# Kernel optimization log

Hardware: AMD Instinct MI355X
Metric: run time of the kernel (lower is better)

Reference implementation:

```python
import jax, jax.numpy as jnp
import numpy as np

TOP_K = 2
N_EXPERTS = 8
ALPHA = 0.1


def setup_inputs() -> dict:
    key = jax.random.key(0)
    k1, k2 = jax.random.split(key)
    hidden_states = jax.random.normal(k1, (4, 8192, 2048), dtype=jnp.float32)
    weight = jax.random.normal(k2, (N_EXPERTS, 2048), dtype=jnp.float32) * (1.0 / np.sqrt(2048))
    return {"hidden_states": hidden_states, "weight": weight}


def reference(hidden_states, weight):
    B, S, H = hidden_states.shape
    E, K = N_EXPERTS, TOP_K
    x = hidden_states.reshape(-1, H)                      # [B*S, H]
    logits = jnp.einsum('th,eh->te', x, weight)           # [B*S, E]
    scores = jax.nn.softmax(logits, axis=-1)
    topk_weight, topk_idx = jax.lax.top_k(scores, K)      # [B*S, K]
    # normalize top-k probs (norm_topk_prob=True, top_k>1)
    topk_weight = topk_weight / (topk_weight.sum(axis=-1, keepdims=True) + 1e-20)
    # seq_aux load-balancing loss (training path)
    idx = topk_idx.reshape(B, S * K)                      # [B, S*K]
    ce = jnp.zeros((B, E), dtype=scores.dtype).at[jnp.arange(B)[:, None], idx].add(1.0)
    ce = ce / (S * K / E)
    pi = scores.reshape(B, S, E).mean(axis=1)             # [B, E]
    aux_loss = (ce * pi).sum(axis=1).mean() * ALPHA
    return topk_idx, topk_weight, aux_loss
```

## Files before the change

kernel.cpp:

```cpp
#include <hip/hip_runtime.h>

#define T_TOK   32768
#define HDIM    2048
#define NEXP    8
#define SEQ     8192
#define NBATCH  4
#define ALPHA   0.1f

#define BLOCK   512
#define TPB     64
#define NBLK    (T_TOK / TPB)
#define H4      (HDIM / 4)
#define NJ      (H4 / 16)

__global__ __launch_bounds__(64) void init_ws_kernel(float* ws) {
    ws[threadIdx.x] = 0.0f;
}

__global__ __launch_bounds__(BLOCK, 4) void gate_kernel(
    const float* __restrict__ x,
    const float* __restrict__ w,
    float* __restrict__ out_idx,
    float* __restrict__ out_wt,
    float* __restrict__ ws)
{
    __shared__ float4 wlds[NEXP * H4];
    __shared__ float sacc[16];

    const int tid  = threadIdx.x;
    const int wid  = tid >> 6;
    const int lane = tid & 63;
    const int grp  = lane >> 4;
    const int col  = lane & 15;

    const float4* w4 = (const float4*)w;
    #pragma unroll
    for (int i = 0; i < 8; ++i)
        wlds[tid + i * BLOCK] = w4[tid + i * BLOCK];
    if (tid < 16) sacc[tid] = 0.0f;
    __syncthreads();

    const int tok0 = blockIdx.x * TPB + wid * 8 + grp * 2;
    const int b    = (blockIdx.x * TPB) / SEQ;

    const float4* xp0 = (const float4*)x + (size_t)tok0 * H4 + col;
    const float4* xp1 = xp0 + H4;

    float acc[2][NEXP];
    #pragma unroll
    for (int t = 0; t < 2; ++t)
        #pragma unroll
        for (int e = 0; e < NEXP; ++e) acc[t][e] = 0.0f;

    float4 xb0[2], xb1[2];
    float4 wA[4], wB[4];

    xb0[0] = xp0[0];        xb0[1] = xp1[0];
    xb1[0] = xp0[16];       xb1[1] = xp1[16];
    #pragma unroll
    for (int e = 0; e < 4; ++e) wA[e] = wlds[e * H4 + col];
    #pragma unroll
    for (int e = 0; e < 4; ++e) wB[e] = wlds[(e + 4) * H4 + col];

#define FMA4(ACC, XV, WV)                      \
    ACC = fmaf((XV).x, (WV).x, ACC);           \
    ACC = fmaf((XV).y, (WV).y, ACC);           \
    ACC = fmaf((XV).z, (WV).z, ACC);           \
    ACC = fmaf((XV).w, (WV).w, ACC);

#define COMPUTE_HALF(XB, WH, EBASE)            \
    _Pragma("unroll")                          \
    for (int e = 0; e < 4; ++e) {              \
        const float4 wv = WH[e];               \
        FMA4(acc[0][(EBASE) + e], XB[0], wv);  \
        FMA4(acc[1][(EBASE) + e], XB[1], wv);  \
    }

    #pragma unroll 1
    for (int jj = 0; jj < NJ - 2; jj += 2) {
        COMPUTE_HALF(xb0, wA, 0)
        #pragma unroll
        for (int e = 0; e < 4; ++e) wA[e] = wlds[e * H4 + (jj + 1) * 16 + col];
        COMPUTE_HALF(xb0, wB, 4)
        #pragma unroll
        for (int e = 0; e < 4; ++e) wB[e] = wlds[(e + 4) * H4 + (jj + 1) * 16 + col];
        xb0[0] = xp0[(jj + 2) * 16];
        xb0[1] = xp1[(jj + 2) * 16];

        COMPUTE_HALF(xb1, wA, 0)
        #pragma unroll
        for (int e = 0; e < 4; ++e) wA[e] = wlds[e * H4 + (jj + 2) * 16 + col];
        COMPUTE_HALF(xb1, wB, 4)
        #pragma unroll
        for (int e = 0; e < 4; ++e) wB[e] = wlds[(e + 4) * H4 + (jj + 2) * 16 + col];
        xb1[0] = xp0[(jj + 3) * 16];
        xb1[1] = xp1[(jj + 3) * 16];
    }

    {
        COMPUTE_HALF(xb0, wA, 0)
        #pragma unroll
        for (int e = 0; e < 4; ++e) wA[e] = wlds[e * H4 + (NJ - 1) * 16 + col];
        COMPUTE_HALF(xb0, wB, 4)
        #pragma unroll
        for (int e = 0; e < 4; ++e) wB[e] = wlds[(e + 4) * H4 + (NJ - 1) * 16 + col];
        COMPUTE_HALF(xb1, wA, 0)
        COMPUTE_HALF(xb1, wB, 4)
    }

    #pragma unroll
    for (int t = 0; t < 2; ++t)
        #pragma unroll
        for (int e = 0; e < NEXP; ++e) {
            float v = acc[t][e];
            v += __shfl_xor(v, 1);
            v += __shfl_xor(v, 2);
            v += __shfl_xor(v, 4);
            v += __shfl_xor(v, 8);
            acc[t][e] = v;
        }

    const int t = col & 1;
    float l[NEXP];
    #pragma unroll
    for (int e = 0; e < NEXP; ++e) l[e] = acc[t][e];

    float mx = l[0];
    #pragma unroll
    for (int e = 1; e < NEXP; ++e) mx = fmaxf(mx, l[e]);

    float p[NEXP];
    float psum = 0.0f;
    #pragma unroll
    for (int e = 0; e < NEXP; ++e) { p[e] = __expf(l[e] - mx); psum += p[e]; }
    const float inv = 1.0f / psum;
    float s[NEXP];
    #pragma unroll
    for (int e = 0; e < NEXP; ++e) s[e] = p[e] * inv;

    float s1 = s[0]; int i1 = 0;
    #pragma unroll
    for (int e = 1; e < NEXP; ++e) if (s[e] > s1) { s1 = s[e]; i1 = e; }
    float s2 = -1.0f; int i2 = 0;
    #pragma unroll
    for (int e = 0; e < NEXP; ++e) if (e != i1 && s[e] > s2) { s2 = s[e]; i2 = e; }

    const float wsum = s1 + s2 + 1e-20f;
    const float w1 = s1 / wsum;
    const float w2 = s2 / wsum;

    if (col < 2) {
        const int tok = tok0 + t;
        ((float2*)out_idx)[tok] = make_float2((float)i1, (float)i2);
        ((float2*)out_wt)[tok]  = make_float2(w1, w2);
    }

    const float sel = (col < 2) ? 1.0f : 0.0f;
    #pragma unroll
    for (int e = 0; e < NEXP; ++e) {
        float pi = s[e] * sel;
        float ce = (((i1 == e) ? 1.0f : 0.0f) + ((i2 == e) ? 1.0f : 0.0f)) * sel;
        pi += __shfl_xor(pi, 1);  ce += __shfl_xor(ce, 1);
        pi += __shfl_xor(pi, 16); ce += __shfl_xor(ce, 16);
        pi += __shfl_xor(pi, 32); ce += __shfl_xor(ce, 32);
        if (lane == 0) {
            atomicAdd(&sacc[e], pi);
            atomicAdd(&sacc[8 + e], ce);
        }
    }
    __syncthreads();
    if (tid < 8)
        atomicAdd(&ws[b * NEXP + tid], sacc[tid]);
    else if (tid < 16)
        atomicAdd(&ws[32 + b * NEXP + (tid - 8)], sacc[tid]);
}

__global__ __launch_bounds__(64) void finalize_kernel(const float* __restrict__ ws,
                                                      float* __restrict__ out_aux) {
    if (threadIdx.x == 0) {
        float aux = 0.0f;
        #pragma unroll
        for (int b = 0; b < NBATCH; ++b) {
            float dot = 0.0f;
            #pragma unroll
            for (int e = 0; e < NEXP; ++e) {
                const float ce = ws[32 + b * NEXP + e] * ((float)NEXP / (float)(SEQ * 2));
                const float pi = ws[b * NEXP + e] / (float)SEQ;
                dot = fmaf(ce, pi, dot);
            }
            aux += dot;
        }
        out_aux[0] = aux * (1.0f / NBATCH) * ALPHA;
    }
}

extern "C" void kernel_launch(void* const* d_in, const int* in_sizes, int n_in,
                              void* d_out, int out_size, void* d_ws, size_t ws_size,
                              hipStream_t stream) {
    const float* x = (const float*)d_in[0];
    const float* w = (const float*)d_in[1];

    float* out     = (float*)d_out;
    float* out_idx = out;
    float* out_wt  = out + 2 * T_TOK;
    float* out_aux = out + 4 * T_TOK;
    float* ws      = (float*)d_ws;

    init_ws_kernel<<<1, 64, 0, stream>>>(ws);
    gate_kernel<<<NBLK, BLOCK, 0, stream>>>(x, w, out_idx, out_wt, ws);
    finalize_kernel<<<1, 64, 0, stream>>>(ws, out_aux);
}
```

Before: 63.51 us.

## Retile gate GEMV to 32 lanes per group with 4 tokens each

```diff
diff --git a/kernel.cpp b/kernel.cpp
--- a/kernel.cpp
+++ b/kernel.cpp
@@ -11,7 +11,7 @@
 #define TPB     64
 #define NBLK    (T_TOK / TPB)
 #define H4      (HDIM / 4)
-#define NJ      (H4 / 16)
+#define NJ2     (H4 / 32)
 
 __global__ __launch_bounds__(64) void init_ws_kernel(float* ws) {
     ws[threadIdx.x] = 0.0f;
@@ -30,8 +30,8 @@
     const int tid  = threadIdx.x;
     const int wid  = tid >> 6;
     const int lane = tid & 63;
-    const int grp  = lane >> 4;
-    const int col  = lane & 15;
+    const int grp  = lane >> 5;
+    const int col  = lane & 31;
 
     const float4* w4 = (const float4*)w;
     #pragma unroll
@@ -40,23 +40,31 @@
     if (tid < 16) sacc[tid] = 0.0f;
     __syncthreads();
 
-    const int tok0 = blockIdx.x * TPB + wid * 8 + grp * 2;
+    const int tok0 = blockIdx.x * TPB + wid * 8 + grp * 4;
     const int b    = (blockIdx.x * TPB) / SEQ;
 
     const float4* xp0 = (const float4*)x + (size_t)tok0 * H4 + col;
     const float4* xp1 = xp0 + H4;
-
-    float acc[2][NEXP];
-    #pragma unroll
-    for (int t = 0; t < 2; ++t)
-        #pragma unroll
-        for (int e = 0; e < NEXP; ++e) acc[t][e] = 0.0f;
-
-    float4 xb0[2], xb1[2];
+    const float4* xp2 = xp0 + 2 * H4;
+    const float4* xp3 = xp0 + 3 * H4;
+
+    float acc[4][NEXP];
+    #pragma unroll
+    for (int m = 0; m < 4; ++m)
+        #pragma unroll
+        for (int e = 0; e < NEXP; ++e) acc[m][e] = 0.0f;
+
+    float4 xb0[4], xb1[4];
     float4 wA[4], wB[4];
 
-    xb0[0] = xp0[0];        xb0[1] = xp1[0];
-    xb1[0] = xp0[16];       xb1[1] = xp1[16];
+#define LOADX(DST, J)                          \
+    DST[0] = xp0[(J) * 32];                    \
+    DST[1] = xp1[(J) * 32];                    \
+    DST[2] = xp2[(J) * 32];                    \
+    DST[3] = xp3[(J) * 32];
+
+    LOADX(xb0, 0)
+    LOADX(xb1, 1)
     #pragma unroll
     for (int e = 0; e < 4; ++e) wA[e] = wlds[e * H4 + col];
     #pragma unroll
@@ -74,53 +82,54 @@
         const float4 wv = WH[e];               \
         FMA4(acc[0][(EBASE) + e], XB[0], wv);  \
         FMA4(acc[1][(EBASE) + e], XB[1], wv);  \
+        FMA4(acc[2][(EBASE) + e], XB[2], wv);  \
+        FMA4(acc[3][(EBASE) + e], XB[3], wv);  \
     }
 
     #pragma unroll 1
-    for (int jj = 0; jj < NJ - 2; jj += 2) {
+    for (int jj = 0; jj < NJ2 - 2; jj += 2) {
         COMPUTE_HALF(xb0, wA, 0)
         #pragma unroll
-        for (int e = 0; e < 4; ++e) wA[e] = wlds[e * H4 + (jj + 1) * 16 + col];
+        for (int e = 0; e < 4; ++e) wA[e] = wlds[e * H4 + (jj + 1) * 32 + col];
         COMPUTE_HALF(xb0, wB, 4)
         #pragma unroll
-        for (int e = 0; e < 4; ++e) wB[e] = wlds[(e + 4) * H4 + (jj + 1) * 16 + col];
-        xb0[0] = xp0[(jj + 2) * 16];
-        xb0[1] = xp1[(jj + 2) * 16];
+        for (int e = 0; e < 4; ++e) wB[e] = wlds[(e + 4) * H4 + (jj + 1) * 32 + col];
+        LOADX(xb0, jj + 2)
 
         COMPUTE_HALF(xb1, wA, 0)
         #pragma unroll
-        for (int e = 0; e < 4; ++e) wA[e] = wlds[e * H4 + (jj + 2) * 16 + col];
+        for (int e = 0; e < 4; ++e) wA[e] = wlds[e * H4 + (jj + 2) * 32 + col];
         COMPUTE_HALF(xb1, wB, 4)
         #pragma unroll
-        for (int e = 0; e < 4; ++e) wB[e] = wlds[(e + 4) * H4 + (jj + 2) * 16 + col];
-        xb1[0] = xp0[(jj + 3) * 16];
-        xb1[1] = xp1[(jj + 3) * 16];
+        for (int e = 0; e < 4; ++e) wB[e] = wlds[(e + 4) * H4 + (jj + 2) * 32 + col];
+        LOADX(xb1, jj + 3)
     }
 
     {
         COMPUTE_HALF(xb0, wA, 0)
         #pragma unroll
-        for (int e = 0; e < 4; ++e) wA[e] = wlds[e * H4 + (NJ - 1) * 16 + col];
+        for (int e = 0; e < 4; ++e) wA[e] = wlds[e * H4 + (NJ2 - 1) * 32 + col];
         COMPUTE_HALF(xb0, wB, 4)
         #pragma unroll
-        for (int e = 0; e < 4; ++e) wB[e] = wlds[(e + 4) * H4 + (NJ - 1) * 16 + col];
+        for (int e = 0; e < 4; ++e) wB[e] = wlds[(e + 4) * H4 + (NJ2 - 1) * 32 + col];
         COMPUTE_HALF(xb1, wA, 0)
         COMPUTE_HALF(xb1, wB, 4)
     }
 
     #pragma unroll
-    for (int t = 0; t < 2; ++t)
+    for (int m = 0; m < 4; ++m)
         #pragma unroll
         for (int e = 0; e < NEXP; ++e) {
-            float v = acc[t][e];
+            float v = acc[m][e];
             v += __shfl_xor(v, 1);
             v += __shfl_xor(v, 2);
             v += __shfl_xor(v, 4);
             v += __shfl_xor(v, 8);
-            acc[t][e] = v;
+            v += __shfl_xor(v, 16);
+            acc[m][e] = v;
         }
 
-    const int t = col & 1;
+    const int t = col & 3;
     float l[NEXP];
     #pragma unroll
     for (int e = 0; e < NEXP; ++e) l[e] = acc[t][e];
@@ -149,19 +158,19 @@
     const float w1 = s1 / wsum;
     const float w2 = s2 / wsum;
 
-    if (col < 2) {
+    if (col < 4) {
         const int tok = tok0 + t;
         ((float2*)out_idx)[tok] = make_float2((float)i1, (float)i2);
         ((float2*)out_wt)[tok]  = make_float2(w1, w2);
     }
 
-    const float sel = (col < 2) ? 1.0f : 0.0f;
+    const float sel = (col < 4) ? 1.0f : 0.0f;
     #pragma unroll
     for (int e = 0; e < NEXP; ++e) {
         float pi = s[e] * sel;
         float ce = (((i1 == e) ? 1.0f : 0.0f) + ((i2 == e) ? 1.0f : 0.0f)) * sel;
         pi += __shfl_xor(pi, 1);  ce += __shfl_xor(ce, 1);
-        pi += __shfl_xor(pi, 16); ce += __shfl_xor(ce, 16);
+        pi += __shfl_xor(pi, 2);  ce += __shfl_xor(ce, 2);
         pi += __shfl_xor(pi, 32); ce += __shfl_xor(ce, 32);
         if (lane == 0) {
             atomicAdd(&sacc[e], pi);
```

New measurement: 182.5 us. 187% more time.

## Replace global atomics with per-block partials and drop workspace init kernel

Applied to the files above, without the earlier changes.

```diff
diff --git a/kernel.cpp b/kernel.cpp
--- a/kernel.cpp
+++ b/kernel.cpp
@@ -10,14 +10,11 @@
 #define BLOCK   512
 #define TPB     64
 #define NBLK    (T_TOK / TPB)
+#define BPB     (SEQ / TPB)
 #define H4      (HDIM / 4)
 #define NJ      (H4 / 16)
 
-__global__ __launch_bounds__(64) void init_ws_kernel(float* ws) {
-    ws[threadIdx.x] = 0.0f;
-}
-
-__global__ __launch_bounds__(BLOCK, 4) void gate_kernel(
+__global__ __launch_bounds__(BLOCK, 2) void gate_kernel(
     const float* __restrict__ x,
     const float* __restrict__ w,
     float* __restrict__ out_idx,
@@ -41,7 +38,6 @@
     __syncthreads();
 
     const int tok0 = blockIdx.x * TPB + wid * 8 + grp * 2;
-    const int b    = (blockIdx.x * TPB) / SEQ;
 
     const float4* xp0 = (const float4*)x + (size_t)tok0 * H4 + col;
     const float4* xp1 = xp0 + H4;
@@ -120,10 +116,11 @@
             acc[t][e] = v;
         }
 
-    const int t = col & 1;
+    const bool selLo = (col & 1) != 0;
     float l[NEXP];
     #pragma unroll
-    for (int e = 0; e < NEXP; ++e) l[e] = acc[t][e];
+    for (int e = 0; e < NEXP; ++e)
+        l[e] = selLo ? acc[1][e] : acc[0][e];
 
     float mx = l[0];
     #pragma unroll
@@ -150,7 +147,7 @@
     const float w2 = s2 / wsum;
 
     if (col < 2) {
-        const int tok = tok0 + t;
+        const int tok = tok0 + (col & 1);
         ((float2*)out_idx)[tok] = make_float2((float)i1, (float)i2);
         ((float2*)out_wt)[tok]  = make_float2(w1, w2);
     }
@@ -169,23 +166,35 @@
         }
     }
     __syncthreads();
-    if (tid < 8)
-        atomicAdd(&ws[b * NEXP + tid], sacc[tid]);
-    else if (tid < 16)
-        atomicAdd(&ws[32 + b * NEXP + (tid - 8)], sacc[tid]);
+    if (tid < 16)
+        ws[blockIdx.x * 16 + tid] = sacc[tid];
 }
 
-__global__ __launch_bounds__(64) void finalize_kernel(const float* __restrict__ ws,
-                                                      float* __restrict__ out_aux) {
-    if (threadIdx.x == 0) {
+__global__ __launch_bounds__(256) void finalize_kernel(const float* __restrict__ ws,
+                                                       float* __restrict__ out_aux) {
+    __shared__ float sfin[NBATCH][16];
+    const int t    = threadIdx.x;
+    const int b    = t >> 6;
+    const int lane = t & 63;
+    const int slot = lane & 15;
+
+    float v = 0.0f;
+    for (int j = lane >> 4; j < BPB; j += 4)
+        v += ws[(b * BPB + j) * 16 + slot];
+    v += __shfl_xor(v, 16);
+    v += __shfl_xor(v, 32);
+    if (lane < 16) sfin[b][slot] = v;
+    __syncthreads();
+
+    if (t == 0) {
         float aux = 0.0f;
         #pragma unroll
-        for (int b = 0; b < NBATCH; ++b) {
+        for (int bb = 0; bb < NBATCH; ++bb) {
             float dot = 0.0f;
             #pragma unroll
             for (int e = 0; e < NEXP; ++e) {
-                const float ce = ws[32 + b * NEXP + e] * ((float)NEXP / (float)(SEQ * 2));
-                const float pi = ws[b * NEXP + e] / (float)SEQ;
+                const float pi = sfin[bb][e] / (float)SEQ;
+                const float ce = sfin[bb][8 + e] * ((float)NEXP / (float)(SEQ * 2));
                 dot = fmaf(ce, pi, dot);
             }
             aux += dot;
@@ -206,7 +215,6 @@
     float* out_aux = out + 4 * T_TOK;
     float* ws      = (float*)d_ws;
 
-    init_ws_kernel<<<1, 64, 0, stream>>>(ws);
     gate_kernel<<<NBLK, BLOCK, 0, stream>>>(x, w, out_idx, out_wt, ws);
-    finalize_kernel<<<1, 64, 0, stream>>>(ws, out_aux);
+    finalize_kernel<<<1, 256, 0, stream>>>(ws, out_aux);
 }
```

Result: slower. 70.97 us (+11.8%).
